# Optimization experiments

Hardware: AMD Instinct MI355X
Metric: run time of the kernel (lower is better)

Reference implementation:

```python
import jax, jax.numpy as jnp
import numpy as np


def setup_inputs() -> dict:
    key = jax.random.key(0)
    k1, k2 = jax.random.split(key)
    B, C, H, W = 8, 64, 32, 32
    K = 8192
    x = jax.random.normal(k1, (B, C, H, W), dtype=jnp.float32)
    codebook = jax.random.normal(k2, (K, C), dtype=jnp.float32)
    return {"x": x, "codebook": codebook}


def reference(x, codebook):
    """Faithful JAX version of VQVAE.quantize().

    x:        [B, C, H, W] latent (output of pre_quant_conv)
    codebook: [K, C] embedding weight
    Returns (quant_out [B,C,H,W], commitment_loss, codebook_loss, indices [B,H,W]).
    """
    B, C, H, W = x.shape
    # [B, H, W, C] -> [B, N, C]
    xf = jnp.transpose(x, (0, 2, 3, 1)).reshape(B, H * W, C)

    # Squared pairwise distances (argmin of cdist == argmin of squared dist).
    x2 = jnp.sum(xf * xf, axis=-1, keepdims=True)            # [B, N, 1]
    e2 = jnp.sum(codebook * codebook, axis=-1)               # [K]
    xe = jnp.einsum('bnc,kc->bnk', xf, codebook)             # [B, N, K]
    d2 = x2 + e2[None, None, :] - 2.0 * xe                   # [B, N, K]
    idx = jnp.argmin(d2, axis=-1)                            # [B, N]

    quant = codebook[idx.reshape(-1)]                        # [B*N, C]
    xflat = xf.reshape(-1, C)                                # [B*N, C]

    commitment_loss = jnp.mean((jax.lax.stop_gradient(quant) - xflat) ** 2)
    codebook_loss = jnp.mean((quant - jax.lax.stop_gradient(xflat)) ** 2)

    # Straight-through estimator.
    quant_st = xflat + jax.lax.stop_gradient(quant - xflat)
    quant_out = jnp.transpose(quant_st.reshape(B, H, W, C), (0, 3, 1, 2))
    indices = idx.reshape(B, H, W)
    return quant_out, commitment_loss, codebook_loss, indices
```

## Files before the change

### kernel.cpp

```cpp
#include <hip/hip_runtime.h>


#define N_PTS   8192
#define K_CODES 8192
#define C_DIM   64
#define HWSZ    1024
#define QOUT_N  524288
#define SPLITS  16

#define WS_XS    0
#define WS_CBS   3145728
#define WS_E2H   6291456
#define WS_PACK  6324224
#define WS_PART  7372800

typedef __attribute__((ext_vector_type(8))) short short8;
typedef __attribute__((ext_vector_type(4))) float floatx4;

__device__ __forceinline__ unsigned short bf16_rne(float f) {
    unsigned u = __float_as_uint(f);
    return (unsigned short)((u + 0x7FFFu + ((u >> 16) & 1u)) >> 16);
}
__device__ __forceinline__ float bf16_val(unsigned short h) {
    return __uint_as_float(((unsigned)h) << 16);
}
__device__ __forceinline__ void split3(float v, unsigned short& h,
                                       unsigned short& m, unsigned short& l) {
    h = bf16_rne(v);
    float r1 = v - bf16_val(h);
    m = bf16_rne(r1);
    float r2 = r1 - bf16_val(m);
    l = bf16_rne(r2);
}

__global__ __launch_bounds__(256)
void vq_prep_kernel(const float* __restrict__ x,
                    const float* __restrict__ cb,
                    unsigned short* __restrict__ xS,
                    unsigned short* __restrict__ cbS,
                    float* __restrict__ e2h)
{
    const int bx  = blockIdx.x;
    const int tid = threadIdx.x;

    if (bx < 32) {
        const int k = bx * 256 + tid;
        const float* row = cb + k * C_DIM;
        float s = 0.0f;
        #pragma unroll
        for (int g = 0; g < 8; ++g) {
            float4 a = *(const float4*)(row + g * 8);
            float4 b = *(const float4*)(row + g * 8 + 4);
            float vv[8] = {a.x, a.y, a.z, a.w, b.x, b.y, b.z, b.w};
            unsigned short h8[8], m8[8], l8[8];
            #pragma unroll
            for (int j = 0; j < 8; ++j) {
                s = fmaf(vv[j], vv[j], s);
                split3(vv[j], h8[j], m8[j], l8[j]);
            }
            *(uint4*)(cbS + ((size_t)(0 * 8 + g) * 8192 + k) * 8) = *(const uint4*)h8;
            *(uint4*)(cbS + ((size_t)(1 * 8 + g) * 8192 + k) * 8) = *(const uint4*)m8;
            *(uint4*)(cbS + ((size_t)(2 * 8 + g) * 8192 + k) * 8) = *(const uint4*)l8;
        }
        e2h[k] = 0.5f * s;
    } else {
        const int u = bx - 32;
        const int b = u >> 3, g = u & 7;
        const float* xb = x + (size_t)(b * C_DIM + g * 8) * HWSZ;
        float v[4][8];
        #pragma unroll
        for (int cq = 0; cq < 8; ++cq) {
            float4 t4 = *(const float4*)(xb + cq * HWSZ + tid * 4);
            v[0][cq] = t4.x; v[1][cq] = t4.y; v[2][cq] = t4.z; v[3][cq] = t4.w;
        }
        #pragma unroll
        for (int j = 0; j < 4; ++j) {
            unsigned short h8[8], m8[8], l8[8];
            #pragma unroll
            for (int cq = 0; cq < 8; ++cq)
                split3(v[j][cq], h8[cq], m8[cq], l8[cq]);
            const size_t n = (size_t)b * 1024 + tid * 4 + j;
            *(uint4*)(xS + ((size_t)(0 * 8 + g) * 8192 + n) * 8) = *(const uint4*)h8;
            *(uint4*)(xS + ((size_t)(1 * 8 + g) * 8192 + n) * 8) = *(const uint4*)m8;
            *(uint4*)(xS + ((size_t)(2 * 8 + g) * 8192 + n) * 8) = *(const uint4*)l8;
        }
    }
}

__device__ __forceinline__ void loadB(const unsigned short* __restrict__ cbS,
                                      const float* __restrict__ e2h,
                                      int code, int quad,
                                      short8 bf[3][2], float& e2v)
{
    #pragma unroll
    for (int p = 0; p < 3; ++p)
        #pragma unroll
        for (int s = 0; s < 2; ++s) {
            int g = s * 4 + quad;
            bf[p][s] = *(const short8*)(cbS + ((size_t)(p * 8 + g) * 8192 + code) * 8);
        }
    e2v = e2h[code];
}

__device__ __forceinline__ void computeTile(const short8 af[4][3][2],
                                            const short8 bf[3][2],
                                            float e2v, int code,
                                            float bestk[4][4], int besti[4][4])
{
    floatx4 acc[4];
    #pragma unroll
    for (int t = 0; t < 4; ++t) acc[t] = (floatx4){0.f, 0.f, 0.f, 0.f};

    #pragma unroll
    for (int s = 0; s < 2; ++s) {
        #pragma unroll
        for (int t = 0; t < 4; ++t)
            acc[t] = __builtin_amdgcn_mfma_f32_16x16x32_bf16(af[t][0][s], bf[0][s], acc[t], 0, 0, 0);
        #pragma unroll
        for (int t = 0; t < 4; ++t)
            acc[t] = __builtin_amdgcn_mfma_f32_16x16x32_bf16(af[t][0][s], bf[1][s], acc[t], 0, 0, 0);
        #pragma unroll
        for (int t = 0; t < 4; ++t)
            acc[t] = __builtin_amdgcn_mfma_f32_16x16x32_bf16(af[t][1][s], bf[0][s], acc[t], 0, 0, 0);
        #pragma unroll
        for (int t = 0; t < 4; ++t)
            acc[t] = __builtin_amdgcn_mfma_f32_16x16x32_bf16(af[t][0][s], bf[2][s], acc[t], 0, 0, 0);
        #pragma unroll
        for (int t = 0; t < 4; ++t)
            acc[t] = __builtin_amdgcn_mfma_f32_16x16x32_bf16(af[t][2][s], bf[0][s], acc[t], 0, 0, 0);
        #pragma unroll
        for (int t = 0; t < 4; ++t)
            acc[t] = __builtin_amdgcn_mfma_f32_16x16x32_bf16(af[t][1][s], bf[1][s], acc[t], 0, 0, 0);
    }

    #pragma unroll
    for (int t = 0; t < 4; ++t)
        #pragma unroll
        for (int r = 0; r < 4; ++r) {
            float key = e2v - acc[t][r];
            bool lt = key < bestk[t][r];
            bestk[t][r] = lt ? key  : bestk[t][r];
            besti[t][r] = lt ? code : besti[t][r];
        }
}

__global__ __launch_bounds__(256, 2)
void vq_argmin_kernel(const unsigned short* __restrict__ xS,
                      const unsigned short* __restrict__ cbS,
                      const float* __restrict__ e2h,
                      unsigned long long* __restrict__ packedS)
{
    __shared__ unsigned long long red[256][17];
    const int tid   = threadIdx.x;
    const int lane  = tid & 63;
    const int w     = tid >> 6;
    const int col   = lane & 15;
    const int quad  = lane >> 4;
    const int mb    = blockIdx.x;
    const int split = blockIdx.y;
    const int m0    = mb * 256 + w * 64;
    const int nb0   = split * 512;

    short8 af[4][3][2];
    #pragma unroll
    for (int t = 0; t < 4; ++t) {
        int pt = m0 + t * 16 + col;
        #pragma unroll
        for (int p = 0; p < 3; ++p)
            #pragma unroll
            for (int s = 0; s < 2; ++s) {
                int g = s * 4 + quad;
                af[t][p][s] = *(const short8*)(xS + ((size_t)(p * 8 + g) * 8192 + pt) * 8);
            }
    }

    float bestk[4][4];
    int   besti[4][4];
    #pragma unroll
    for (int t = 0; t < 4; ++t)
        #pragma unroll
        for (int r = 0; r < 4; ++r) {
            bestk[t][r] = __uint_as_float(0x7F800000u);
            besti[t][r] = 0;
        }

    short8 b0[3][2], b1[3][2];
    float  e0, e1;
    loadB(cbS, e2h, nb0 + col, quad, b0, e0);

    for (int nt = 0; nt < 32; nt += 2) {
        loadB(cbS, e2h, nb0 + (nt + 1) * 16 + col, quad, b1, e1);
        computeTile(af, b0, e0, nb0 + nt * 16 + col, bestk, besti);
        if (nt + 2 < 32)
            loadB(cbS, e2h, nb0 + (nt + 2) * 16 + col, quad, b0, e0);
        computeTile(af, b1, e1, nb0 + (nt + 1) * 16 + col, bestk, besti);
    }

    #pragma unroll
    for (int t = 0; t < 4; ++t)
        #pragma unroll
        for (int r = 0; r < 4; ++r) {
            unsigned u = __float_as_uint(bestk[t][r]);
            u = ((int)u < 0) ? ~u : (u | 0x80000000u);
            unsigned long long p = ((unsigned long long)u << 32) | (unsigned)besti[t][r];
            red[w * 64 + t * 16 + quad * 4 + r][col] = p;
        }
    __syncthreads();
    unsigned long long v = red[tid][0];
    #pragma unroll
    for (int c = 1; c < 16; ++c) {
        unsigned long long q = red[tid][c];
        v = (q < v) ? q : v;
    }
    packedS[split * N_PTS + mb * 256 + tid] = v;
}

__global__ __launch_bounds__(256)
void vq_gather_kernel(const float* __restrict__ x,
                      const float* __restrict__ cb,
                      const unsigned long long* __restrict__ packedS,
                      float* __restrict__ out,
                      float* __restrict__ part)
{
    const int t = blockIdx.x * 256 + threadIdx.x;
    const int n  = t & (N_PTS - 1);
    const int qd = t >> 13;
    const int c0 = qd * 16;

    unsigned long long v = packedS[n];
    #pragma unroll
    for (int s = 1; s < SPLITS; ++s) {
        unsigned long long q = packedS[s * N_PTS + n];
        v = (q < v) ? q : v;
    }
    const unsigned idx = (unsigned)(v & 0xFFFFFFFFull);

    const int b  = n >> 10;
    const int hw = n & 1023;
    const float* xb = x   + (size_t)b * (C_DIM * HWSZ) + hw;
    float*       ob = out + (size_t)b * (C_DIM * HWSZ) + hw;

    float s = 0.0f;
    #pragma unroll
    for (int c4 = 0; c4 < 4; ++c4) {
        float4 q = *(const float4*)(cb + (size_t)idx * C_DIM + c0 + c4 * 4);
        float qa[4] = {q.x, q.y, q.z, q.w};
        #pragma unroll
        for (int j = 0; j < 4; ++j) {
            int c = c0 + c4 * 4 + j;
            float xv = xb[c * HWSZ];
            float d  = qa[j] - xv;
            s = fmaf(d, d, s);
            ob[c * HWSZ] = xv + d;
        }
    }

    if (qd == 0) out[QOUT_N + 2 + n] = (float)idx;

    #pragma unroll
    for (int off = 32; off > 0; off >>= 1) s += __shfl_down(s, off, 64);
    if ((threadIdx.x & 63) == 0) part[t >> 6] = s;
}

__global__ __launch_bounds__(256)
void vq_final_kernel(const float* __restrict__ part, float* __restrict__ out)
{
    __shared__ float w[4];
    float s = part[threadIdx.x] + part[threadIdx.x + 256];
    #pragma unroll
    for (int off = 32; off > 0; off >>= 1) s += __shfl_down(s, off, 64);
    if ((threadIdx.x & 63) == 0) w[threadIdx.x >> 6] = s;
    __syncthreads();
    if (threadIdx.x == 0) {
        float m = (w[0] + w[1] + w[2] + w[3]) * (1.0f / (float)QOUT_N);
        out[QOUT_N]     = m;
        out[QOUT_N + 1] = m;
    }
}

extern "C" void kernel_launch(void* const* d_in, const int* in_sizes, int n_in,
                              void* d_out, int out_size, void* d_ws, size_t ws_size,
                              hipStream_t stream)
{
    const float* x  = (const float*)d_in[0];
    const float* cb = (const float*)d_in[1];
    float* out = (float*)d_out;
    char*  ws  = (char*)d_ws;
    (void)ws_size;

    unsigned short* xS  = (unsigned short*)(ws + WS_XS);
    unsigned short* cbS = (unsigned short*)(ws + WS_CBS);
    float* e2h = (float*)(ws + WS_E2H);
    unsigned long long* packedS = (unsigned long long*)(ws + WS_PACK);
    float* part = (float*)(ws + WS_PART);

    vq_prep_kernel<<<96, 256, 0, stream>>>(x, cb, xS, cbS, e2h);
    vq_argmin_kernel<<<dim3(N_PTS / 256, SPLITS), 256, 0, stream>>>(xS, cbS, e2h, packedS);
    vq_gather_kernel<<<128, 256, 0, stream>>>(x, cb, packedS, out, part);
    vq_final_kernel<<<1, 256, 0, stream>>>(part, out);
}
```

Baseline: 105.3 us.

## Double codebook splits, fold -e2 into MFMA accumulator init, dedupe gather argmin

Doubles the number of codebook splits so each argmin block scans 256 codes instead of 512, and raises the occupancy hint in launch bounds from 2 to 4 blocks per CU. The aim is more parallel blocks and better latency hiding. The -|e|^2 term now initialises the MFMA accumulator, which removes a subtraction per element, and the search becomes an argmax of the score. The gather kernel reduces across splits once per point into shared memory instead of once per thread in each of four channel groups, offsetting the larger partial array.

```diff
diff --git a/kernel.cpp b/kernel.cpp
--- a/kernel.cpp
+++ b/kernel.cpp
@@ -6,13 +6,13 @@
 #define C_DIM   64
 #define HWSZ    1024
 #define QOUT_N  524288
-#define SPLITS  16
+#define SPLITS  32
 
 #define WS_XS    0
 #define WS_CBS   3145728
 #define WS_E2H   6291456
 #define WS_PACK  6324224
-#define WS_PART  7372800
+#define WS_PART  8421376
 
 typedef __attribute__((ext_vector_type(8))) short short8;
 typedef __attribute__((ext_vector_type(4))) float floatx4;
@@ -90,7 +90,7 @@
 __device__ __forceinline__ void loadB(const unsigned short* __restrict__ cbS,
                                       const float* __restrict__ e2h,
                                       int code, int quad,
-                                      short8 bf[3][2], float& e2v)
+                                      short8 bf[3][2], float& me2)
 {
     #pragma unroll
     for (int p = 0; p < 3; ++p)
@@ -99,17 +99,17 @@
             int g = s * 4 + quad;
             bf[p][s] = *(const short8*)(cbS + ((size_t)(p * 8 + g) * 8192 + code) * 8);
         }
-    e2v = e2h[code];
+    me2 = -e2h[code];
 }
 
 __device__ __forceinline__ void computeTile(const short8 af[4][3][2],
                                             const short8 bf[3][2],
-                                            float e2v, int code,
-                                            float bestk[4][4], int besti[4][4])
+                                            float me2, int code,
+                                            float bestv[4][4], int besti[4][4])
 {
     floatx4 acc[4];
     #pragma unroll
-    for (int t = 0; t < 4; ++t) acc[t] = (floatx4){0.f, 0.f, 0.f, 0.f};
+    for (int t = 0; t < 4; ++t) acc[t] = (floatx4){me2, me2, me2, me2};
 
     #pragma unroll
     for (int s = 0; s < 2; ++s) {
@@ -137,14 +137,14 @@
     for (int t = 0; t < 4; ++t)
         #pragma unroll
         for (int r = 0; r < 4; ++r) {
-            float key = e2v - acc[t][r];
-            bool lt = key < bestk[t][r];
-            bestk[t][r] = lt ? key  : bestk[t][r];
-            besti[t][r] = lt ? code : besti[t][r];
-        }
-}
-
-__global__ __launch_bounds__(256, 2)
+            float sc = acc[t][r];
+            bool gt = sc > bestv[t][r];
+            bestv[t][r] = gt ? sc   : bestv[t][r];
+            besti[t][r] = gt ? code : besti[t][r];
+        }
+}
+
+__global__ __launch_bounds__(256, 4)
 void vq_argmin_kernel(const unsigned short* __restrict__ xS,
                       const unsigned short* __restrict__ cbS,
                       const float* __restrict__ e2h,
@@ -159,7 +159,7 @@
     const int mb    = blockIdx.x;
     const int split = blockIdx.y;
     const int m0    = mb * 256 + w * 64;
-    const int nb0   = split * 512;
+    const int nb0   = split * 256;
 
     short8 af[4][3][2];
     #pragma unroll
@@ -174,13 +174,13 @@
             }
     }
 
-    float bestk[4][4];
+    float bestv[4][4];
     int   besti[4][4];
     #pragma unroll
     for (int t = 0; t < 4; ++t)
         #pragma unroll
         for (int r = 0; r < 4; ++r) {
-            bestk[t][r] = __uint_as_float(0x7F800000u);
+            bestv[t][r] = __uint_as_float(0xFF800000u);
             besti[t][r] = 0;
         }
 
@@ -188,19 +188,19 @@
     float  e0, e1;
     loadB(cbS, e2h, nb0 + col, quad, b0, e0);
 
-    for (int nt = 0; nt < 32; nt += 2) {
+    for (int nt = 0; nt < 16; nt += 2) {
         loadB(cbS, e2h, nb0 + (nt + 1) * 16 + col, quad, b1, e1);
-        computeTile(af, b0, e0, nb0 + nt * 16 + col, bestk, besti);
-        if (nt + 2 < 32)
+        computeTile(af, b0, e0, nb0 + nt * 16 + col, bestv, besti);
+        if (nt + 2 < 16)
             loadB(cbS, e2h, nb0 + (nt + 2) * 16 + col, quad, b0, e0);
-        computeTile(af, b1, e1, nb0 + (nt + 1) * 16 + col, bestk, besti);
+        computeTile(af, b1, e1, nb0 + (nt + 1) * 16 + col, bestv, besti);
     }
 
     #pragma unroll
     for (int t = 0; t < 4; ++t)
         #pragma unroll
         for (int r = 0; r < 4; ++r) {
-            unsigned u = __float_as_uint(bestk[t][r]);
+            unsigned u = __float_as_uint(-bestv[t][r]);
             u = ((int)u < 0) ? ~u : (u | 0x80000000u);
             unsigned long long p = ((unsigned long long)u << 32) | (unsigned)besti[t][r];
             red[w * 64 + t * 16 + quad * 4 + r][col] = p;
@@ -212,7 +212,7 @@
         unsigned long long q = red[tid][c];
         v = (q < v) ? q : v;
     }
-    packedS[split * N_PTS + mb * 256 + tid] = v;
+    packedS[(size_t)split * N_PTS + mb * 256 + tid] = v;
 }
 
 __global__ __launch_bounds__(256)
@@ -222,21 +222,30 @@
                       float* __restrict__ out,
                       float* __restrict__ part)
 {
-    const int t = blockIdx.x * 256 + threadIdx.x;
-    const int n  = t & (N_PTS - 1);
-    const int qd = t >> 13;
-    const int c0 = qd * 16;
-
-    unsigned long long v = packedS[n];
-    #pragma unroll
-    for (int s = 1; s < SPLITS; ++s) {
-        unsigned long long q = packedS[s * N_PTS + n];
-        v = (q < v) ? q : v;
-    }
-    const unsigned idx = (unsigned)(v & 0xFFFFFFFFull);
-
-    const int b  = n >> 10;
-    const int hw = n & 1023;
+    __shared__ int sidx[64];
+    const int tid  = threadIdx.x;
+    const int lane = tid & 63;
+    const int qd   = tid >> 6;
+    const int n0   = blockIdx.x * 64;
+    const int n    = n0 + lane;
+
+    if (qd == 0) {
+        unsigned long long v = packedS[n];
+        #pragma unroll
+        for (int s = 1; s < SPLITS; ++s) {
+            unsigned long long q = packedS[(size_t)s * N_PTS + n];
+            v = (q < v) ? q : v;
+        }
+        int idx = (int)(v & 0xFFFFFFFFull);
+        sidx[lane] = idx;
+        out[QOUT_N + 2 + n] = (float)idx;
+    }
+    __syncthreads();
+
+    const int idx = sidx[lane];
+    const int c0  = qd * 16;
+    const int b   = n >> 10;
+    const int hw  = n & 1023;
     const float* xb = x   + (size_t)b * (C_DIM * HWSZ) + hw;
     float*       ob = out + (size_t)b * (C_DIM * HWSZ) + hw;
 
@@ -255,11 +264,9 @@
         }
     }
 
-    if (qd == 0) out[QOUT_N + 2 + n] = (float)idx;
-
     #pragma unroll
     for (int off = 32; off > 0; off >>= 1) s += __shfl_down(s, off, 64);
-    if ((threadIdx.x & 63) == 0) part[t >> 6] = s;
+    if (lane == 0) part[blockIdx.x * 4 + qd] = s;
 }
 
 __global__ __launch_bounds__(256)
```

Result: slower. 363.6 us (+245.3%).
